# Optimization experiments

Hardware: AMD Instinct MI355X
Metric: run time of the kernel (lower is better)

## Reference

```python
import jax, jax.numpy as jnp
import numpy as np

T, C, H, D = 4096, 1024, 16, 64

def setup_inputs() -> dict:
    key = jax.random.key(0)
    ks = jax.random.split(key, 6)
    s = 0.02
    return {
        "tokens": jax.random.normal(ks[0], (T, C), jnp.float32),
        "Wq": jax.random.normal(ks[1], (H, C, D), jnp.float32) * s,
        "Wk": jax.random.normal(ks[2], (H, C, D), jnp.float32) * s,
        "Wv": jax.random.normal(ks[3], (H, C, D), jnp.float32) * s,
        "Wp": jax.random.normal(ks[4], (H * D, C), jnp.float32) * s,
        "bp": jnp.zeros((C,), jnp.float32),
    }

def reference(tokens, Wq, Wk, Wv, Wp, bp):
    # per-head projections: [H, T, D]
    q = jnp.einsum("tc,hcd->htd", tokens, Wq)
    k = jnp.einsum("tc,hcd->htd", tokens, Wk)
    v = jnp.einsum("tc,hcd->htd", tokens, Wv)
    # attention scores [H, T, T], causal mask, stable softmax
    wei = jnp.einsum("htd,hsd->hts", q, k) / jnp.sqrt(jnp.float32(D))
    causal = jnp.tril(jnp.ones((T, T), dtype=bool))
    wei = jnp.where(causal, wei, -jnp.inf)
    wei = jax.nn.softmax(wei, axis=-1)
    attn = jnp.einsum("hts,hsd->htd", wei, v)
    # concat heads -> [T, H*D] (head-major order matches torch-style concat)
    out = attn.transpose(1, 0, 2).reshape(T, H * D)
    return out @ Wp + bp
```

## Files before the change

kernel.cpp:

```cpp
#include <hip/hip_runtime.h>
#include <hip/hip_bf16.h>
#include <stdint.h>

#define T_DIM 4096
#define C_DIM 1024
#define HD    1024

typedef unsigned short u16;

using bf16x8 = __attribute__((ext_vector_type(8))) short;
using bf16x4 = __attribute__((ext_vector_type(4))) short;
using f32x4  = __attribute__((ext_vector_type(4))) float;

#define MFMA16(a, b, c) __builtin_amdgcn_mfma_f32_16x16x32_bf16(a, b, c, 0, 0, 0)

#define ALPHA 0.18033688011112042f

__device__ __forceinline__ u16 f2bf(float f) {
  union { __hip_bfloat16 h; u16 u; } cv;
  cv.h = __float2bfloat16(f);
  return cv.u;
}

__device__ __forceinline__ void load_lds16(const u16* g, u16* l) {
  __builtin_amdgcn_global_load_lds(
      (const __attribute__((address_space(1))) unsigned int*)g,
      (__attribute__((address_space(3))) unsigned int*)l, 16, 0, 0);
}


__global__ void k_pack(const float* __restrict__ tokens,
                       const float* __restrict__ Wq, const float* __restrict__ Wk,
                       const float* __restrict__ Wv, const float* __restrict__ Wp,
                       u16* __restrict__ tok_b, u16* __restrict__ Wt, u16* __restrict__ Wpt) {
  __shared__ float Tsm[64][65];
  int bx = blockIdx.x;
  int t = threadIdx.x;
  if (bx < 4096) {
    int i = (bx * 256 + t) * 4;
    float4 v = *(const float4*)(tokens + i);
    bf16x4 o = { (short)f2bf(v.x), (short)f2bf(v.y), (short)f2bf(v.z), (short)f2bf(v.w) };
    *(bf16x4*)(tok_b + i) = o;
    return;
  }
  if (bx < 4864) {
    int b = bx - 4096;
    int qkv = b >> 8;
    int h = (b >> 4) & 15;
    int c0 = (b & 15) << 6;
    const float* W = (qkv == 0) ? Wq : ((qkv == 1) ? Wk : Wv);
    const float* src = W + (size_t)h * 65536 + (size_t)c0 * 64;
#pragma unroll
    for (int i = 0; i < 4; ++i) {
      int fl = i * 256 + t;
      int r = fl >> 4, c4 = fl & 15;
      float4 v = *(const float4*)(src + r * 64 + c4 * 4);
      Tsm[r][c4 * 4 + 0] = v.x; Tsm[r][c4 * 4 + 1] = v.y;
      Tsm[r][c4 * 4 + 2] = v.z; Tsm[r][c4 * 4 + 3] = v.w;
    }
    __syncthreads();
    int d = t >> 2, seg = t & 3;
    bf16x8 o0, o1;
#pragma unroll
    for (int j = 0; j < 8; ++j) o0[j] = (short)f2bf(Tsm[seg * 16 + j][d]);
#pragma unroll
    for (int j = 0; j < 8; ++j) o1[j] = (short)f2bf(Tsm[seg * 16 + 8 + j][d]);
    u16* dst = Wt + (size_t)(qkv * 1024 + h * 64 + d) * 1024 + c0 + seg * 16;
    *(bf16x8*)dst = o0;
    *(bf16x8*)(dst + 8) = o1;
    return;
  }
  {
    int b = bx - 4864;
    int k0 = (b >> 4) << 6;
    int co0 = (b & 15) << 6;
#pragma unroll
    for (int i = 0; i < 4; ++i) {
      int fl = i * 256 + t;
      int r = fl >> 4, c4 = fl & 15;
      float4 v = *(const float4*)(Wp + (size_t)(k0 + r) * 1024 + co0 + c4 * 4);
      Tsm[r][c4 * 4 + 0] = v.x; Tsm[r][c4 * 4 + 1] = v.y;
      Tsm[r][c4 * 4 + 2] = v.z; Tsm[r][c4 * 4 + 3] = v.w;
    }
    __syncthreads();
    int d = t >> 2, seg = t & 3;
    bf16x8 o0, o1;
#pragma unroll
    for (int j = 0; j < 8; ++j) o0[j] = (short)f2bf(Tsm[seg * 16 + j][d]);
#pragma unroll
    for (int j = 0; j < 8; ++j) o1[j] = (short)f2bf(Tsm[seg * 16 + 8 + j][d]);
    u16* dst = Wpt + (size_t)(co0 + d) * 1024 + k0 + seg * 16;
    *(bf16x8*)dst = o0;
    *(bf16x8*)(dst + 8) = o1;
  }
}


template<int MODE>
__global__ __launch_bounds__(256, 3) void k_gemm(
    const u16* __restrict__ A, const u16* __restrict__ B, int K,
    u16* __restrict__ Qb, u16* __restrict__ Kb, u16* __restrict__ Vt,
    float* __restrict__ Cout, const float* __restrict__ bias)
{
  __shared__ u16 Asm[3][128 * 32];
  __shared__ u16 Bsm[3][128 * 32];
  const int tid = threadIdx.x;
  const int lane = tid & 63, wid = tid >> 6;
  const int g = lane >> 4, lq = lane & 15;

  int flat = blockIdx.y * gridDim.x + blockIdx.x;
  int nwg = gridDim.x * gridDim.y;
  int sw = (flat & 7) * (nwg >> 3) + (flat >> 3);
  const int m0 = (sw / gridDim.x) * 128, n0 = (sw % gridDim.x) * 128;
  const int wm = wid >> 1, wn = wid & 1;

  const f32x4 z4 = {0.f, 0.f, 0.f, 0.f};
  f32x4 acc[4][4];
#pragma unroll
  for (int m = 0; m < 4; ++m)
#pragma unroll
    for (int n = 0; n < 4; ++n) acc[m][n] = z4;

  auto stage = [&](int k0, int buf) {
#pragma unroll
    for (int i = 0; i < 2; ++i) {
      int ch = i * 256 + tid;
      int r = ch >> 2, cp = ch & 3, cd = cp ^ ((r >> 1) & 3);
      load_lds16(A + (size_t)(m0 + r) * K + k0 + cd * 8, &Asm[buf][ch * 8]);
      load_lds16(B + (size_t)(n0 + r) * K + k0 + cd * 8, &Bsm[buf][ch * 8]);
    }
  };

  const int nk = K >> 5;
  stage(0, 0);
  stage(32, 1);
  asm volatile("s_waitcnt vmcnt(4)" ::: "memory");

  const int sx = (lq >> 1) & 3;
  int cbuf = 0;
  for (int it = 0; it < nk; ++it) {
    __builtin_amdgcn_s_barrier();
    if (it + 2 < nk) {
      int sbuf = cbuf + 2; if (sbuf >= 3) sbuf -= 3;
      stage((it + 2) << 5, sbuf);
    }

    bf16x8 af[4], bfr[4];
#pragma unroll
    for (int m = 0; m < 4; ++m)
      af[m] = *(const bf16x8*)&Asm[cbuf][(wm * 64 + m * 16 + lq) * 32 + ((g ^ sx) << 3)];
#pragma unroll
    for (int n = 0; n < 4; ++n)
      bfr[n] = *(const bf16x8*)&Bsm[cbuf][(wn * 64 + n * 16 + lq) * 32 + ((g ^ sx) << 3)];
#pragma unroll
    for (int m = 0; m < 4; ++m)
#pragma unroll
      for (int n = 0; n < 4; ++n)
        acc[m][n] = MFMA16(af[m], bfr[n], acc[m][n]);

    if (it + 2 < nk) asm volatile("s_waitcnt vmcnt(4) lgkmcnt(0)" ::: "memory");
    else             asm volatile("s_waitcnt vmcnt(0) lgkmcnt(0)" ::: "memory");
    cbuf = cbuf + 1; if (cbuf == 3) cbuf = 0;
  }

  if (MODE == 0) {
    const int region = n0 >> 10;
#pragma unroll
    for (int m = 0; m < 4; ++m) {
      int t0 = m0 + wm * 64 + m * 16 + 4 * g;
#pragma unroll
      for (int n = 0; n < 4; ++n) {
        int j = n0 + wn * 64 + n * 16 + lq;
        if (region == 0) {
#pragma unroll
          for (int r = 0; r < 4; ++r)
            Qb[(size_t)(t0 + r) * HD + j] = f2bf(acc[m][n][r] * ALPHA);
        } else if (region == 1) {
#pragma unroll
          for (int r = 0; r < 4; ++r) Kb[(size_t)(t0 + r) * HD + (j - 1024)] = f2bf(acc[m][n][r]);
        } else {
          bf16x4 pv = { (short)f2bf(acc[m][n][0]), (short)f2bf(acc[m][n][1]),
                        (short)f2bf(acc[m][n][2]), (short)f2bf(acc[m][n][3]) };
          *(bf16x4*)&Vt[(size_t)(j - 2048) * T_DIM + t0] = pv;
        }
      }
    }
  } else {
#pragma unroll
    for (int m = 0; m < 4; ++m) {
      int t0 = m0 + wm * 64 + m * 16 + 4 * g;
#pragma unroll
      for (int n = 0; n < 4; ++n) {
        int j = n0 + wn * 64 + n * 16 + lq;
        float bv = bias[j];
#pragma unroll
        for (int r = 0; r < 4; ++r)
          Cout[(size_t)(t0 + r) * C_DIM + j] = acc[m][n][r] + bv;
      }
    }
  }
}


#define SLOTS_PER_H 80

__global__ __launch_bounds__(256, 3) void k_attn(
    const u16* __restrict__ Qb, const u16* __restrict__ Kb,
    const u16* __restrict__ Vt, u16* __restrict__ Ob,
    float* __restrict__ PU, float* __restrict__ Pl)
{
  __shared__ u16 Ksm[3][64 * 64];
  __shared__ u16 Vsm[3][64 * 64];
  const int tid = threadIdx.x;
  const int lane = tid & 63, w = tid >> 6;
  const int g = lane >> 4, lq = lane & 15;

  int bx = blockIdx.x;
  int xcd = bx & 7, ul = bx >> 3;
  int h, qi, c;
  if (ul < 96) {
    int hp = ul / 48, k = ul % 48;
    if (k < 8)       { qi = 8 + k;               c = 0; }
    else if (k < 24) { int j = k - 8;  qi = 16 + (j >> 1); c = j & 1; }
    else             { int j = k - 24; qi = 24 + j / 3;    c = j % 3; }
    h = xcd * 2 + hp;
  } else {
    int v = ul - 96;
    int hp = v >> 5, k = v & 31;
    int m = 7 - (k >> 2), band = k & 3;
    qi = band * 8 + m; c = band;
    h = xcd * 2 + hp;
  }
  const int a = qi >> 3;
  const int slot = h * SLOTS_PER_H + qi + 4 * a * (a - 1) + a * (qi & 7) + c;

  const int Q0 = qi << 7;
  const int qwave = Q0 + w * 32;
  const int st = c << 4;
  const int et = min((qi + 1) * 2, st + 16);

  bf16x8 qf[2][2];
#pragma unroll
  for (int qs = 0; qs < 2; ++qs) {
    const u16* qp = Qb + (size_t)(qwave + qs * 16 + lq) * HD + h * 64;
    qf[qs][0] = *(const bf16x8*)(qp + g * 8);
    qf[qs][1] = *(const bf16x8*)(qp + 32 + g * 8);
  }
  bf16x8 ones8;
#pragma unroll
  for (int j = 0; j < 8; ++j) ones8[j] = (short)0x3F80;

  const f32x4 z4 = {0.f, 0.f, 0.f, 0.f};
  f32x4 accO[2][4];
  f32x4 accL[2];
#pragma unroll
  for (int qs = 0; qs < 2; ++qs) {
    accL[qs] = z4;
#pragma unroll
    for (int n = 0; n < 4; ++n) accO[qs][n] = z4;
  }

  auto stage = [&](int kvs, int buf) {
#pragma unroll
    for (int i = 0; i < 2; ++i) {
      int ch = i * 256 + tid;
      int r = ch >> 3, cp = ch & 7, cd = cp ^ (r & 7);
      load_lds16(Kb + (size_t)(kvs + r) * HD + h * 64 + cd * 8, &Ksm[buf][ch * 8]);
    }
#pragma unroll
    for (int i = 0; i < 2; ++i) {
      int ch = i * 256 + tid;
      int r = ch >> 3, cp = ch & 7, cd = cp ^ (r & 7);
      load_lds16(Vt + (size_t)(h * 64 + r) * T_DIM + kvs + cd * 8, &Vsm[buf][ch * 8]);
    }
  };

  stage(st << 6, 0);
  stage((st + 1) << 6, 1);
  asm volatile("s_waitcnt vmcnt(4)" ::: "memory");

  int cbuf = 0;
  for (int it = st; it < et; ++it) {
    __builtin_amdgcn_s_barrier();
    if (it + 2 < et) {
      int sbuf = cbuf + 2; if (sbuf >= 3) sbuf -= 3;
      stage((it + 2) << 6, sbuf);
    }

    const int kv0 = it << 6;
    if (kv0 <= qwave + 31) {
      f32x4 s[2][4];
#pragma unroll
      for (int ks = 0; ks < 4; ++ks) {
        const int kvl = ks * 16 + lq;
        const u16* kr = &Ksm[cbuf][kvl * 64];
        bf16x8 kf0 = *(const bf16x8*)(kr + ((g ^ (kvl & 7)) << 3));
        bf16x8 kf1 = *(const bf16x8*)(kr + (((4 + g) ^ (kvl & 7)) << 3));
        s[0][ks] = MFMA16(kf0, qf[0][0], z4);
        s[0][ks] = MFMA16(kf1, qf[0][1], s[0][ks]);
        s[1][ks] = MFMA16(kf0, qf[1][0], z4);
        s[1][ks] = MFMA16(kf1, qf[1][1], s[1][ks]);
      }

      if (kv0 + 63 > qwave) {
#pragma unroll
        for (int qs = 0; qs < 2; ++qs) {
          int qa = qwave + qs * 16 + lq;
#pragma unroll
          for (int ks = 0; ks < 4; ++ks)
#pragma unroll
            for (int r = 0; r < 4; ++r) {
              int kva = kv0 + ks * 16 + 4 * g + r;
              float sv = (kva > qa) ? -1e30f : s[qs][ks][r];
              s[qs][ks][r] = __builtin_amdgcn_exp2f(sv);
            }
        }
      } else {
#pragma unroll
        for (int qs = 0; qs < 2; ++qs)
#pragma unroll
          for (int ks = 0; ks < 4; ++ks)
#pragma unroll
            for (int r = 0; r < 4; ++r)
              s[qs][ks][r] = __builtin_amdgcn_exp2f(s[qs][ks][r]);
      }

      bf16x8 pa[2][2];
#pragma unroll
      for (int qs = 0; qs < 2; ++qs) {
        pa[qs][0] = { (short)f2bf(s[qs][0][0]), (short)f2bf(s[qs][0][1]),
                      (short)f2bf(s[qs][0][2]), (short)f2bf(s[qs][0][3]),
                      (short)f2bf(s[qs][1][0]), (short)f2bf(s[qs][1][1]),
                      (short)f2bf(s[qs][1][2]), (short)f2bf(s[qs][1][3]) };
        pa[qs][1] = { (short)f2bf(s[qs][2][0]), (short)f2bf(s[qs][2][1]),
                      (short)f2bf(s[qs][2][2]), (short)f2bf(s[qs][2][3]),
                      (short)f2bf(s[qs][3][0]), (short)f2bf(s[qs][3][1]),
                      (short)f2bf(s[qs][3][2]), (short)f2bf(s[qs][3][3]) };
      }

      accL[0] = MFMA16(pa[0][0], ones8, accL[0]);
      accL[0] = MFMA16(pa[0][1], ones8, accL[0]);
      accL[1] = MFMA16(pa[1][0], ones8, accL[1]);
      accL[1] = MFMA16(pa[1][1], ones8, accL[1]);

#pragma unroll
      for (int n = 0; n < 4; ++n) {
        const int d = n * 16 + lq;
        const u16* vr = &Vsm[cbuf][d * 64];
        const int xo = d & 7;
        const int go = (g & 1) * 4;
        bf16x4 lo0 = *(const bf16x4*)(vr + ((((g >> 1) + 0) ^ xo) << 3) + go);
        bf16x4 hi0 = *(const bf16x4*)(vr + ((((g >> 1) + 2) ^ xo) << 3) + go);
        bf16x4 lo1 = *(const bf16x4*)(vr + ((((g >> 1) + 4) ^ xo) << 3) + go);
        bf16x4 hi1 = *(const bf16x4*)(vr + ((((g >> 1) + 6) ^ xo) << 3) + go);
        bf16x8 vf0 = __builtin_shufflevector(lo0, hi0, 0, 1, 2, 3, 4, 5, 6, 7);
        bf16x8 vf1 = __builtin_shufflevector(lo1, hi1, 0, 1, 2, 3, 4, 5, 6, 7);
        accO[0][n] = MFMA16(pa[0][0], vf0, accO[0][n]);
        accO[0][n] = MFMA16(pa[0][1], vf1, accO[0][n]);
        accO[1][n] = MFMA16(pa[1][0], vf0, accO[1][n]);
        accO[1][n] = MFMA16(pa[1][1], vf1, accO[1][n]);
      }
    }

    if (it + 2 < et) asm volatile("s_waitcnt vmcnt(4) lgkmcnt(0)" ::: "memory");
    else             asm volatile("s_waitcnt vmcnt(0) lgkmcnt(0)" ::: "memory");
    cbuf = cbuf + 1; if (cbuf == 3) cbuf = 0;
  }

  if (a == 0) {
#pragma unroll
    for (int qs = 0; qs < 2; ++qs) {
      float inv[4];
#pragma unroll
      for (int r = 0; r < 4; ++r) inv[r] = __builtin_amdgcn_rcpf(accL[qs][r]);
      int qrow = qwave + qs * 16 + 4 * g;
#pragma unroll
      for (int n = 0; n < 4; ++n) {
        int dcol = h * 64 + n * 16 + lq;
#pragma unroll
        for (int r = 0; r < 4; ++r)
          Ob[(size_t)(qrow + r) * HD + dcol] = f2bf(accO[qs][n][r] * inv[r]);
      }
    }
  } else {
#pragma unroll
    for (int qs = 0; qs < 2; ++qs) {
      if (lq == 0) {
#pragma unroll
        for (int r = 0; r < 4; ++r)
          Pl[(size_t)slot * 128 + w * 32 + qs * 16 + 4 * g + r] = accL[qs][r];
      }
#pragma unroll
      for (int n = 0; n < 4; ++n) {
#pragma unroll
        for (int r = 0; r < 4; ++r)
          PU[(size_t)slot * 8192 + (size_t)(w * 32 + qs * 16 + 4 * g + r) * 64 + n * 16 + lq]
              = accO[qs][n][r];
      }
    }
  }
}


__global__ void k_combine(const float* __restrict__ PU, const float* __restrict__ Pl,
                          u16* __restrict__ Ob) {
  int b = blockIdx.x;
  int h = b / 24;
  int qi = 8 + (b % 24);
  int a = qi >> 3, nch = a + 1;
  int slot0 = h * SLOTS_PER_H + qi + 4 * a * (a - 1) + a * (qi & 7);
  int t = threadIdx.x;
  int r = t >> 1, half = t & 1;

  float L = 0.f;
#pragma unroll
  for (int c = 0; c < 4; ++c)
    if (c < nch) L += Pl[(size_t)(slot0 + c) * 128 + r];

  float o[32];
#pragma unroll
  for (int j = 0; j < 32; ++j) o[j] = 0.f;
#pragma unroll
  for (int c = 0; c < 4; ++c) {
    if (c < nch) {
      const float4* up = (const float4*)(PU + (size_t)(slot0 + c) * 8192 + r * 64 + half * 32);
#pragma unroll
      for (int j = 0; j < 8; ++j) {
        float4 u = up[j];
        o[4*j+0] += u.x; o[4*j+1] += u.y;
        o[4*j+2] += u.z; o[4*j+3] += u.w;
      }
    }
  }
  float inv = 1.f / L;
  bf16x8 ov[4];
#pragma unroll
  for (int j = 0; j < 32; ++j) ov[j >> 3][j & 7] = (short)f2bf(o[j] * inv);
  u16* dst = Ob + (size_t)(qi * 128 + r) * HD + h * 64 + half * 32;
#pragma unroll
  for (int v = 0; v < 4; ++v) *(bf16x8*)(dst + v * 8) = ov[v];
}


extern "C" void kernel_launch(void* const* d_in, const int* in_sizes, int n_in,
                              void* d_out, int out_size, void* d_ws, size_t ws_size,
                              hipStream_t stream) {
  const float* tokens = (const float*)d_in[0];
  const float* Wq = (const float*)d_in[1];
  const float* Wk = (const float*)d_in[2];
  const float* Wv = (const float*)d_in[3];
  const float* Wp = (const float*)d_in[4];
  const float* bp = (const float*)d_in[5];
  float* out = (float*)d_out;

  char* w = (char*)d_ws;
  u16* tok_b = (u16*)w; w += (size_t)T_DIM * C_DIM * 2;
  u16* Ob    = tok_b;
  u16* Wt    = (u16*)w; w += (size_t)3072 * C_DIM * 2;
  u16* Wpt   = (u16*)w; w += (size_t)1024 * C_DIM * 2;
  u16* Qb    = (u16*)w; w += (size_t)T_DIM * HD * 2;
  u16* Kb    = (u16*)w; w += (size_t)T_DIM * HD * 2;
  u16* Vt    = (u16*)w; w += (size_t)T_DIM * HD * 2;
  float* PU  = (float*)w; w += (size_t)16 * SLOTS_PER_H * 8192 * 4;
  float* Pl  = (float*)w; w += (size_t)16 * SLOTS_PER_H * 128 * 4;

  k_pack<<<5120, 256, 0, stream>>>(tokens, Wq, Wk, Wv, Wp, tok_b, Wt, Wpt);

  k_gemm<0><<<dim3(24, 32), 256, 0, stream>>>(tok_b, Wt, 1024, Qb, Kb, Vt, nullptr, nullptr);
  k_attn<<<1280, 256, 0, stream>>>(Qb, Kb, Vt, Ob, PU, Pl);
  k_combine<<<384, 256, 0, stream>>>(PU, Pl, Ob);
  k_gemm<1><<<dim3(8, 32), 256, 0, stream>>>(Ob, Wpt, 1024, nullptr, nullptr, nullptr, out, bp);
}
```

Measured before the change: 206.8 us.

## Rebalance attention split-KV chunking to 12-tile chunks and add MFMA priority hints

Changes the split-KV work decomposition in the attention kernel from 16-tile chunks to 12-tile chunks, giving 1632 work items with a new slot mapping, and updates the combine kernel to sum up to six partials. It also raises wave priority around the MFMA sections with s_setprio, and coarsens the token-packing blocks so each handles four float4 strips. The aim is better load balance and tail behaviour across CUs and less scheduling overhead. In exchange there are more partial writes and reads through the PU workspace, plus extra combine work.

```diff
diff --git a/kernel.cpp b/kernel.cpp
--- a/kernel.cpp
+++ b/kernel.cpp
@@ -36,15 +36,18 @@
   __shared__ float Tsm[64][65];
   int bx = blockIdx.x;
   int t = threadIdx.x;
-  if (bx < 4096) {
-    int i = (bx * 256 + t) * 4;
-    float4 v = *(const float4*)(tokens + i);
-    bf16x4 o = { (short)f2bf(v.x), (short)f2bf(v.y), (short)f2bf(v.z), (short)f2bf(v.w) };
-    *(bf16x4*)(tok_b + i) = o;
+  if (bx < 1024) {
+#pragma unroll
+    for (int j = 0; j < 4; ++j) {
+      int i = ((bx * 4 + j) * 256 + t) * 4;
+      float4 v = *(const float4*)(tokens + i);
+      bf16x4 o = { (short)f2bf(v.x), (short)f2bf(v.y), (short)f2bf(v.z), (short)f2bf(v.w) };
+      *(bf16x4*)(tok_b + i) = o;
+    }
     return;
   }
-  if (bx < 4864) {
-    int b = bx - 4096;
+  if (bx < 1792) {
+    int b = bx - 1024;
     int qkv = b >> 8;
     int h = (b >> 4) & 15;
     int c0 = (b & 15) << 6;
@@ -71,7 +74,7 @@
     return;
   }
   {
-    int b = bx - 4864;
+    int b = bx - 1792;
     int k0 = (b >> 4) << 6;
     int co0 = (b & 15) << 6;
 #pragma unroll
@@ -202,7 +205,7 @@
 }
 
 
-#define SLOTS_PER_H 80
+#define SLOTS_PER_H 96
 
 __global__ __launch_bounds__(256, 3) void k_attn(
     const u16* __restrict__ Qb, const u16* __restrict__ Kb,
@@ -217,27 +220,20 @@
 
   int bx = blockIdx.x;
   int xcd = bx & 7, ul = bx >> 3;
-  int h, qi, c;
-  if (ul < 96) {
-    int hp = ul / 48, k = ul % 48;
-    if (k < 8)       { qi = 8 + k;               c = 0; }
-    else if (k < 24) { int j = k - 8;  qi = 16 + (j >> 1); c = j & 1; }
-    else             { int j = k - 24; qi = 24 + j / 3;    c = j % 3; }
-    h = xcd * 2 + hp;
-  } else {
-    int v = ul - 96;
-    int hp = v >> 5, k = v & 31;
-    int m = 7 - (k >> 2), band = k & 3;
-    qi = band * 8 + m; c = band;
-    h = xcd * 2 + hp;
-  }
-  const int a = qi >> 3;
-  const int slot = h * SLOTS_PER_H + qi + 4 * a * (a - 1) + a * (qi & 7) + c;
+  int hp = ul & 1, u = ul >> 1;
+  int qi, c;
+  if (u < 12)       { qi = 30 + u / 6;          c = u % 6; }
+  else if (u < 42)  { int v = u - 12; qi = 24 + v / 5; c = v % 5; }
+  else if (u < 66)  { int v = u - 42; qi = 18 + v / 4; c = v % 4; }
+  else if (u < 84)  { int v = u - 66; qi = 12 + v / 3; c = v % 3; }
+  else if (u < 96)  { int v = u - 84; qi = 6 + v / 2;  c = v % 2; }
+  else              { qi = u - 96;              c = 0; }
+  const int h = xcd * 2 + hp;
 
   const int Q0 = qi << 7;
   const int qwave = Q0 + w * 32;
-  const int st = c << 4;
-  const int et = min((qi + 1) * 2, st + 16);
+  const int st = c * 12;
+  const int et = min((qi + 1) * 2, st + 12);
 
   bf16x8 qf[2][2];
 #pragma unroll
@@ -290,6 +286,7 @@
     const int kv0 = it << 6;
     if (kv0 <= qwave + 31) {
       f32x4 s[2][4];
+      __builtin_amdgcn_s_setprio(1);
 #pragma unroll
       for (int ks = 0; ks < 4; ++ks) {
         const int kvl = ks * 16 + lq;
@@ -301,6 +298,7 @@
         s[1][ks] = MFMA16(kf0, qf[1][0], z4);
         s[1][ks] = MFMA16(kf1, qf[1][1], s[1][ks]);
       }
+      __builtin_amdgcn_s_setprio(0);
 
       if (kv0 + 63 > qwave) {
 #pragma unroll
@@ -338,6 +336,7 @@
                       (short)f2bf(s[qs][3][2]), (short)f2bf(s[qs][3][3]) };
       }
 
+      __builtin_amdgcn_s_setprio(1);
       accL[0] = MFMA16(pa[0][0], ones8, accL[0]);
       accL[0] = MFMA16(pa[0][1], ones8, accL[0]);
       accL[1] = MFMA16(pa[1][0], ones8, accL[1]);
@@ -360,6 +359,7 @@
         accO[1][n] = MFMA16(pa[1][0], vf0, accO[1][n]);
         accO[1][n] = MFMA16(pa[1][1], vf1, accO[1][n]);
       }
+      __builtin_amdgcn_s_setprio(0);
     }
 
     if (it + 2 < et) asm volatile("s_waitcnt vmcnt(4) lgkmcnt(0)" ::: "memory");
@@ -367,7 +367,7 @@
     cbuf = cbuf + 1; if (cbuf == 3) cbuf = 0;
   }
 
-  if (a == 0) {
+  if (qi < 6) {
 #pragma unroll
     for (int qs = 0; qs < 2; ++qs) {
       float inv[4];
@@ -383,6 +383,8 @@
       }
     }
   } else {
+    int bb = qi / 6, rr = qi % 6;
+    int slot = h * SLOTS_PER_H + 3 * bb * (bb + 1) - 6 + rr * (bb + 1) + c;
 #pragma unroll
     for (int qs = 0; qs < 2; ++qs) {
       if (lq == 0) {
@@ -405,23 +407,24 @@
 __global__ void k_combine(const float* __restrict__ PU, const float* __restrict__ Pl,
                           u16* __restrict__ Ob) {
   int b = blockIdx.x;
-  int h = b / 24;
-  int qi = 8 + (b % 24);
-  int a = qi >> 3, nch = a + 1;
-  int slot0 = h * SLOTS_PER_H + qi + 4 * a * (a - 1) + a * (qi & 7);
+  int h = b / 26;
+  int qi = 6 + (b % 26);
+  int bb = qi / 6, rr = qi % 6;
+  int nch = bb + 1;
+  int slot0 = h * SLOTS_PER_H + 3 * bb * (bb + 1) - 6 + rr * (bb + 1);
   int t = threadIdx.x;
   int r = t >> 1, half = t & 1;
 
   float L = 0.f;
 #pragma unroll
-  for (int c = 0; c < 4; ++c)
+  for (int c = 0; c < 6; ++c)
     if (c < nch) L += Pl[(size_t)(slot0 + c) * 128 + r];
 
   float o[32];
 #pragma unroll
   for (int j = 0; j < 32; ++j) o[j] = 0.f;
 #pragma unroll
-  for (int c = 0; c < 4; ++c) {
+  for (int c = 0; c < 6; ++c) {
     if (c < nch) {
       const float4* up = (const float4*)(PU + (size_t)(slot0 + c) * 8192 + r * 64 + half * 32);
 #pragma unroll
@@ -464,10 +467,10 @@
   float* PU  = (float*)w; w += (size_t)16 * SLOTS_PER_H * 8192 * 4;
   float* Pl  = (float*)w; w += (size_t)16 * SLOTS_PER_H * 128 * 4;
 
-  k_pack<<<5120, 256, 0, stream>>>(tokens, Wq, Wk, Wv, Wp, tok_b, Wt, Wpt);
+  k_pack<<<2048, 256, 0, stream>>>(tokens, Wq, Wk, Wv, Wp, tok_b, Wt, Wpt);
 
   k_gemm<0><<<dim3(24, 32), 256, 0, stream>>>(tok_b, Wt, 1024, Qb, Kb, Vt, nullptr, nullptr);
-  k_attn<<<1280, 256, 0, stream>>>(Qb, Kb, Vt, Ob, PU, Pl);
-  k_combine<<<384, 256, 0, stream>>>(PU, Pl, Ob);
+  k_attn<<<1632, 256, 0, stream>>>(Qb, Kb, Vt, Ob, PU, Pl);
+  k_combine<<<416, 256, 0, stream>>>(PU, Pl, Ob);
   k_gemm<1><<<dim3(8, 32), 256, 0, stream>>>(Ob, Wpt, 1024, nullptr, nullptr, nullptr, out, bp);
 }
```

Result: no change. 206.5 us (-0.2%).
